# Performance work log

Measured on AMD Instinct MI355X. Metric: run time of the kernel, lower is better.

The kernel has to match this reference:

```python
import jax, jax.numpy as jnp
import numpy as np

HEADS = 16
HIDDEN = 1024
HEAD_DIM = HIDDEN // HEADS


def setup_inputs() -> dict:
    key = jax.random.key(0)
    ks = jax.random.split(key, 12)
    B, S, H = 2, 2048, HIDDEN
    scale = 1.0 / np.sqrt(H)
    inp = {
        'q': jax.random.normal(ks[0], (B, S, H), jnp.float32),
        'k': jax.random.normal(ks[1], (B, S, H), jnp.float32),
        'v': jax.random.normal(ks[2], (B, S, H), jnp.float32),
        'mask': jnp.ones((B, S), jnp.int32),
        'Wq': jax.random.normal(ks[3], (H, H), jnp.float32) * scale,
        'bq': jnp.zeros((H,), jnp.float32),
        'Wk': jax.random.normal(ks[4], (H, H), jnp.float32) * scale,
        'bk': jnp.zeros((H,), jnp.float32),
        'Wv': jax.random.normal(ks[5], (H, H), jnp.float32) * scale,
        'bv': jnp.zeros((H,), jnp.float32),
        'Wo': jax.random.normal(ks[6], (H, H), jnp.float32) * scale,
        'bo': jnp.zeros((H,), jnp.float32),
    }
    return inp


def reference(q, k, v, mask, Wq, bq, Wk, bk, Wv, bv, Wo, bo):
    B, S, H = q.shape
    hd = HEAD_DIM
    # projections (torch Linear: x @ W.T + b) -> [B, heads, S, hd]
    qh = (q @ Wq.T + bq).reshape(B, S, HEADS, hd).transpose(0, 2, 1, 3)
    kh = (k @ Wk.T + bk).reshape(B, S, HEADS, hd).transpose(0, 2, 1, 3)
    vh = (v @ Wv.T + bv).reshape(B, S, HEADS, hd).transpose(0, 2, 1, 3)
    # full score matrix [B, heads, Sq, Sk]
    scores = jnp.einsum('bhqd,bhkd->bhqk', qh, kh) / np.sqrt(hd)
    # mask [B, Sq] -> [B, 1, Sq, 1], masks entire query rows where mask==0
    m = mask[:, None, :, None]
    scores = jnp.where(m == 0, jnp.float32(-1e9), scores)
    attn = jax.nn.softmax(scores, axis=-1)
    # dropout omitted (eval mode / deterministic)
    y = jnp.einsum('bhqk,bhkd->bhqd', attn, vh)
    y = y.transpose(0, 2, 1, 3).reshape(B, S, H)
    return y @ Wo.T + bo
```

## Files before the change

kernel.cpp:

```cpp
#include <hip/hip_runtime.h>
#include <hip/hip_bf16.h>
#include <cstdint>

#define EL 1048576ull

typedef __bf16 bf16_t;
typedef bf16_t bf16x8 __attribute__((ext_vector_type(8)));
typedef float  f32x4  __attribute__((ext_vector_type(4)));
typedef unsigned int u32x2 __attribute__((ext_vector_type(2)));
typedef unsigned int u32x4 __attribute__((ext_vector_type(4)));

__device__ __forceinline__ unsigned short f2bf(float f) {
  unsigned int u = __builtin_bit_cast(unsigned int, f);
  u += 0x7FFFu + ((u >> 16) & 1u);
  return (unsigned short)(u >> 16);
}

__device__ __forceinline__ unsigned int cvtpk(float lo, float hi2) {
  unsigned int r;
  asm("v_cvt_pk_bf16_f32 %0, %1, %2" : "=v"(r) : "v"(lo), "v"(hi2));
  return r;
}

__device__ __forceinline__ float fexp2(float x) {
#if __has_builtin(__builtin_amdgcn_exp2f)
  return __builtin_amdgcn_exp2f(x);
#else
  return exp2f(x);
#endif
}

typedef __attribute__((address_space(1))) void as1_void;
typedef __attribute__((address_space(3))) void as3_void;
__device__ __forceinline__ void load_lds16(const void* g, void* l) {
  __builtin_amdgcn_global_load_lds((as1_void*)g, (as3_void*)l, 16, 0, 0);
}

__device__ __forceinline__ bf16x8 repack_af(const f32x4 s0v, const f32x4 s1v) {
  unsigned int c00 = cvtpk(s0v[0], s0v[1]);
  unsigned int c01 = cvtpk(s0v[2], s0v[3]);
  unsigned int c10 = cvtpk(s1v[0], s1v[1]);
  unsigned int c11 = cvtpk(s1v[2], s1v[3]);
  asm("v_permlane32_swap_b32 %0, %1" : "+v"(c00), "+v"(c10));
  asm("v_permlane16_swap_b32 %0, %1" : "+v"(c00), "+v"(c10));
  asm("v_permlane32_swap_b32 %0, %1" : "+v"(c01), "+v"(c11));
  asm("v_permlane16_swap_b32 %0, %1" : "+v"(c01), "+v"(c11));
  u32x4 wd; wd[0] = c00; wd[1] = c01; wd[2] = c10; wd[3] = c11;
  return __builtin_bit_cast(bf16x8, wd);
}

__global__ __launch_bounds__(256) void convert_all(
    const float* __restrict__ q, const float* __restrict__ k, const float* __restrict__ v,
    const float* __restrict__ wq, const float* __restrict__ wk,
    const float* __restrict__ wv, const float* __restrict__ wo,
    unsigned short* __restrict__ ws)
{
  const size_t total_v4 = 4 * EL;
  for (size_t v4 = (size_t)blockIdx.x * blockDim.x + threadIdx.x; v4 < total_v4;
       v4 += (size_t)gridDim.x * blockDim.x) {
    size_t e = v4 * 4;
    unsigned seg = (unsigned)(e >> 20);
    const float* s; size_t base;
    if      (seg < 4)   { s = q;  base = 0; }
    else if (seg < 8)   { s = k;  base = 4*EL; }
    else if (seg < 12)  { s = v;  base = 8*EL; }
    else if (seg == 12) { s = wq; base = 12*EL; }
    else if (seg == 13) { s = wk; base = 13*EL; }
    else if (seg == 14) { s = wv; base = 14*EL; }
    else                { s = wo; base = 15*EL; }
    const float4 f = *(const float4*)(s + (e - base));
    ushort4 o;
    o.x = f2bf(f.x); o.y = f2bf(f.y); o.z = f2bf(f.z); o.w = f2bf(f.w);
    *(ushort4*)(ws + e) = o;
  }
}

template <int BM, int BN, int WM, int WN>
__device__ __forceinline__ void gemm_bt_main(
    const unsigned short* __restrict__ A,
    const unsigned short* __restrict__ B,
    f32x4 (&acc)[BM / WM / 16][BN / WN / 16],
    const int tm, const int tn)
{
  constexpr int K = 1024, BK = 64;
  constexpr int AM = BM / WM / 16, AN = BN / WN / 16;
  __shared__ __align__(16) unsigned short sA[BM * BK];
  __shared__ __align__(16) unsigned short sB[BN * BK];
  const int tid  = threadIdx.x;
  const int wave = tid >> 6, lane = tid & 63;
  const int wm = wave / WN, wn = wave % WN;
  const int l16 = lane & 15, hi = lane >> 4, swz = l16 & 7;

  for (int k0 = 0; k0 < K; k0 += BK) {
    __syncthreads();
#pragma unroll
    for (int i = 0; i < BM * 8 / 256; i++) {
      int p = i * 256 + tid;
      int row = p >> 3, c = p & 7;
      load_lds16(A + (size_t)(tm + row) * K + k0 + ((c ^ (row & 7)) * 8),
                 &sA[(i * 256 + wave * 64) * 8]);
    }
#pragma unroll
    for (int i = 0; i < BN * 8 / 256; i++) {
      int p = i * 256 + tid;
      int row = p >> 3, c = p & 7;
      load_lds16(B + (size_t)(tn + row) * K + k0 + ((c ^ (row & 7)) * 8),
                 &sB[(i * 256 + wave * 64) * 8]);
    }
    __syncthreads();

#pragma unroll
    for (int kk = 0; kk < 2; kk++) {
      bf16x8 af[AM], bfr[AN];
#pragma unroll
      for (int i = 0; i < AM; i++) {
        int row = wm * (BM / WM) + i * 16 + l16;
        af[i] = *(const bf16x8*)&sA[row * BK + (((kk * 4 + hi) ^ swz) * 8)];
      }
#pragma unroll
      for (int j = 0; j < AN; j++) {
        int row = wn * (BN / WN) + j * 16 + l16;
        bfr[j] = *(const bf16x8*)&sB[row * BK + (((kk * 4 + hi) ^ swz) * 8)];
      }
#pragma unroll
      for (int i = 0; i < AM; i++)
#pragma unroll
        for (int j = 0; j < AN; j++)
          acc[i][j] = __builtin_amdgcn_mfma_f32_16x16x32_bf16(af[i], bfr[j], acc[i][j], 0, 0, 0);
    }
  }
}

__global__ __launch_bounds__(256, 3) void qkv_gemm(
    const unsigned short* qb, const unsigned short* kb, const unsigned short* vb,
    const unsigned short* wqb, const unsigned short* wkb, const unsigned short* wvb,
    const float* bq, const float* bk, const float* bv,
    unsigned short* Qp, unsigned short* Kp, unsigned short* Vt)
{
  const unsigned short* A; const unsigned short* B; const float* bias;
  if (blockIdx.z == 0)      { A = qb; B = wqb; bias = bq; }
  else if (blockIdx.z == 1) { A = kb; B = wkb; bias = bk; }
  else                      { A = vb; B = wvb; bias = bv; }

  const int xd = blockIdx.x, yd = blockIdx.y;
  const int mt = xd + 8 * (yd & 3);
  const int nt = yd >> 2;
  const int tm = mt * 128, tn = nt * 128;

  f32x4 acc[4][4] = {};
  gemm_bt_main<128, 128, 2, 2>(A, B, acc, tm, tn);

  const int tid = threadIdx.x, wave = tid >> 6, lane = tid & 63;
  const int wm = wave >> 1, wn = wave & 1;
  const int l16 = lane & 15, hi = lane >> 4;

  if (blockIdx.z < 2) {
    unsigned short* C = (blockIdx.z == 0) ? Qp : Kp;
    const float scale = (blockIdx.z == 0) ? 0.18033688011112042f : 1.0f;
#pragma unroll
    for (int i = 0; i < 4; i++) {
      int row0 = tm + wm * 64 + i * 16 + hi * 4;
#pragma unroll
      for (int j = 0; j < 4; j++) {
        int col = tn + wn * 64 + j * 16 + l16;
        float bv2 = bias[col];
#pragma unroll
        for (int r = 0; r < 4; r++)
          C[(size_t)(row0 + r) * 1024 + col] = f2bf((acc[i][j][r] + bv2) * scale);
      }
    }
  } else {
#pragma unroll
    for (int i = 0; i < 4; i++) {
      int row0 = tm + wm * 64 + i * 16 + hi * 4;
      int bb = row0 >> 11, s = row0 & 2047;
#pragma unroll
      for (int j = 0; j < 4; j++) {
        int col = tn + wn * 64 + j * 16 + l16;
        int hh = col >> 6, d = col & 63;
        float bv2 = bias[col];
        u32x2 w;
        w[0] = cvtpk(acc[i][j][0] + bv2, acc[i][j][1] + bv2);
        w[1] = cvtpk(acc[i][j][2] + bv2, acc[i][j][3] + bv2);
        *(u32x2*)&Vt[((size_t)(bb * 16 + hh) * 64 + d) * 2048 + s] = w;
      }
    }
  }
}

__global__ __launch_bounds__(256, 2) void out_gemm(
    const unsigned short* Yb, const unsigned short* wob, const float* bo, float* out)
{
  const int xd = blockIdx.x, yd = blockIdx.y;
  const int mt = (xd & 7) + 8 * (yd & 3);
  const int nt = (xd >> 3) + 2 * (yd >> 2);
  const int tm = mt * 128, tn = nt * 64;

  f32x4 acc[2][4] = {};
  gemm_bt_main<128, 64, 4, 1>(Yb, wob, acc, tm, tn);

  const int tid = threadIdx.x, wave = tid >> 6, lane = tid & 63;
  const int l16 = lane & 15, hi = lane >> 4;
#pragma unroll
  for (int i = 0; i < 2; i++) {
    int row0 = tm + wave * 32 + i * 16 + hi * 4;
#pragma unroll
    for (int j = 0; j < 4; j++) {
      int col = tn + j * 16 + l16;
      float bv2 = bo[col];
#pragma unroll
      for (int r = 0; r < 4; r++)
        out[(size_t)(row0 + r) * 1024 + col] = acc[i][j][r] + bv2;
    }
  }
}

__global__ __launch_bounds__(512, 2) void attn_kernel(
    const unsigned short* __restrict__ Qp, const unsigned short* __restrict__ Kp,
    const unsigned short* __restrict__ Vt, const int* __restrict__ mask,
    unsigned short* __restrict__ Yb)
{
  constexpr int S = 2048, H = 1024;
  __shared__ __align__(16) unsigned short smem[32768];

  const int tid = threadIdx.x, wave = tid >> 6, lane = tid & 63;
  const int l16 = lane & 15, hi = lane >> 4, swz = l16 & 7;
  const int half = wave >> 2, w4 = wave & 3;
  const int kvoff = half * 1024;
  const int xd = blockIdx.x, hd = blockIdx.y;
  const int h  = (xd & 7) + 8 * (hd & 1);
  const int qt = ((xd >> 3) + 2 * (hd >> 1)) * 128;
  const int b = blockIdx.z, bh = b * 16 + h;
  const unsigned short* Qb = Qp + (size_t)b * S * H + (size_t)h * 64;
  const unsigned short* Kb = Kp + (size_t)b * S * H + (size_t)h * 64;
  const unsigned short* Vb = Vt + (size_t)bh * 64 * 2048;

  unsigned short* sK0 = smem + (half * 2) * 4096;
  unsigned short* sK1 = smem + (half * 2 + 1) * 4096;
  unsigned short* sV0 = smem + 16384 + (half * 2) * 4096;
  unsigned short* sV1 = smem + 16384 + (half * 2 + 1) * 4096;

  const int kinv0 = l16 * 64 + ((hi ^ swz) * 8);
  const int kinv1 = l16 * 64 + (((4 + hi) ^ swz) * 8);
  const int vinv0 = kinv0, vinv1 = kinv1;

  {
    unsigned short* qdst0 = smem + 4096;
    unsigned short* qdst1 = smem + 12288;
#pragma unroll
    for (int i = 0; i < 2; i++) {
      int p = i * 512 + tid, row = p >> 3, c = p & 7;
      load_lds16(Qb + (size_t)(qt + row) * H + ((c ^ (row & 7)) * 8),
                 &(i ? qdst1 : qdst0)[(wave * 64) * 8]);
    }
  }
  const int htid = tid & 255;
  const unsigned short* pK[2]; const unsigned short* pV[2];
#pragma unroll
  for (int j = 0; j < 2; j++) {
    int g = j * 256 + htid;
    int row = g >> 3, c = g & 7;
    pK[j] = Kb + (size_t)(kvoff + row) * H + ((c ^ (row & 7)) * 8);
    int d = g >> 3, kvc = g & 7;
    int sg = kvc ^ (d & 7);
    pV[j] = Vb + (size_t)d * 2048 + kvoff + sg * 8;
  }
#pragma unroll
  for (int j = 0; j < 2; j++)
    load_lds16(pK[j], &sK0[(j * 256 + w4 * 64) * 8]);
#pragma unroll
  for (int j = 0; j < 2; j++)
    load_lds16(pV[j], &sV0[(j * 256 + w4 * 64) * 8]);
#pragma unroll
  for (int j = 0; j < 2; j++) { pK[j] += 64 * H; pV[j] += 64; }

  asm volatile("s_waitcnt vmcnt(4)" ::: "memory");
  __builtin_amdgcn_sched_barrier(0);
  __builtin_amdgcn_s_barrier();

  bf16x8 qf[2][2];
#pragma unroll
  for (int m = 0; m < 2; m++) {
    const int row = w4 * 32 + m * 16 + l16;
    const int qm = mask[(size_t)b * S + qt + row];
    const unsigned short* qsrc = (row < 64) ? (smem + 4096 + row * 64)
                                            : (smem + 12288 + (row - 64) * 64);
#pragma unroll
    for (int ks = 0; ks < 2; ks++) {
      bf16x8 v = *(const bf16x8*)&qsrc[((ks * 4 + hi) ^ swz) * 8];
      u32x4 u = __builtin_bit_cast(u32x4, v);
#pragma unroll
      for (int c = 0; c < 4; c++) u[c] = qm ? u[c] : 0u;
      qf[m][ks] = __builtin_bit_cast(bf16x8, u);
    }
  }
  asm volatile("s_waitcnt lgkmcnt(0)" ::: "memory");
  __builtin_amdgcn_sched_barrier(0);

  float lsum[2] = {0.f, 0.f};
  f32x4 oacc[2][4] = {};

  for (int t = 0; t < 16; t++) {
    const int cur = t & 1;
    asm volatile("s_waitcnt vmcnt(0)" ::: "memory");
    __builtin_amdgcn_sched_barrier(0);
    __builtin_amdgcn_s_barrier();

    if (t < 15) {
      unsigned short* nK = cur ? sK0 : sK1;
      unsigned short* nV = cur ? sV0 : sV1;
#pragma unroll
      for (int j = 0; j < 2; j++)
        load_lds16(pK[j], &nK[(j * 256 + w4 * 64) * 8]);
#pragma unroll
      for (int j = 0; j < 2; j++)
        load_lds16(pV[j], &nV[(j * 256 + w4 * 64) * 8]);
#pragma unroll
      for (int j = 0; j < 2; j++) { pK[j] += 64 * H; pV[j] += 64; }
    }

    const unsigned short* kb = cur ? sK1 : sK0;
    const unsigned short* vb = cur ? sV1 : sV0;

    f32x4 sf[2][4];
    __builtin_amdgcn_s_setprio(1);
#pragma unroll
    for (int jj = 0; jj < 4; jj++) {
      const int ro = jj * 1024;
      bf16x8 kf0 = *(const bf16x8*)&kb[ro + kinv0];
      bf16x8 kf1 = *(const bf16x8*)&kb[ro + kinv1];
#pragma unroll
      for (int m = 0; m < 2; m++) {
        f32x4 acc = {-16.0f, -16.0f, -16.0f, -16.0f};
        acc = __builtin_amdgcn_mfma_f32_16x16x32_bf16(kf0, qf[m][0], acc, 0, 0, 0);
        acc = __builtin_amdgcn_mfma_f32_16x16x32_bf16(kf1, qf[m][1], acc, 0, 0, 0);
        sf[m][jj] = acc;
      }
    }
    __builtin_amdgcn_s_setprio(0);

#pragma unroll
    for (int m = 0; m < 2; m++) {
#pragma unroll
      for (int jj = 0; jj < 4; jj++)
#pragma unroll
        for (int r = 0; r < 4; r++)
          sf[m][jj][r] = fexp2(sf[m][jj][r]);
      f32x4 c4 = (sf[m][0] + sf[m][1]) + (sf[m][2] + sf[m][3]);
      lsum[m] += (c4[0] + c4[1]) + (c4[2] + c4[3]);
    }

#pragma unroll
    for (int w2 = 0; w2 < 2; w2++) {
      bf16x8 af0 = repack_af(sf[0][2 * w2], sf[0][2 * w2 + 1]);
      bf16x8 af1 = repack_af(sf[1][2 * w2], sf[1][2 * w2 + 1]);
      const int vo = w2 ? vinv1 : vinv0;
      __builtin_amdgcn_s_setprio(1);
#pragma unroll
      for (int n = 0; n < 4; n++) {
        bf16x8 vf = *(const bf16x8*)&vb[n * 1024 + vo];
        oacc[0][n] = __builtin_amdgcn_mfma_f32_16x16x32_bf16(af0, vf, oacc[0][n], 0, 0, 0);
        oacc[1][n] = __builtin_amdgcn_mfma_f32_16x16x32_bf16(af1, vf, oacc[1][n], 0, 0, 0);
      }
      __builtin_amdgcn_s_setprio(0);
    }
  }

#pragma unroll
  for (int m = 0; m < 2; m++) {
    lsum[m] += __shfl_xor(lsum[m], 16);
    lsum[m] += __shfl_xor(lsum[m], 32);
  }

  __syncthreads();

  float* sO = (float*)smem;
  float* sL = (float*)(smem + 16896);

  if (half == 1) {
#pragma unroll
    for (int m = 0; m < 2; m++) {
      if (hi == 0) sL[w4 * 32 + m * 16 + l16] = lsum[m];
#pragma unroll
      for (int n = 0; n < 4; n++)
#pragma unroll
        for (int r = 0; r < 4; r++) {
          int qq = w4 * 32 + m * 16 + hi * 4 + r;
          sO[qq * 66 + n * 16 + l16] = oacc[m][n][r];
        }
    }
  }
  __syncthreads();
  if (half == 0) {
#pragma unroll
    for (int m = 0; m < 2; m++) {
      float lt = lsum[m] + sL[w4 * 32 + m * 16 + l16];
      float lr[4];
#pragma unroll
      for (int r = 0; r < 4; r++) lr[r] = 1.0f / __shfl(lt, hi * 4 + r);
#pragma unroll
      for (int n = 0; n < 4; n++)
#pragma unroll
        for (int r = 0; r < 4; r++) {
          int qq = w4 * 32 + m * 16 + hi * 4 + r;
          int col = n * 16 + l16;
          float val = (oacc[m][n][r] + sO[qq * 66 + col]) * lr[r];
          Yb[((size_t)b * S + qt + qq) * H + h * 64 + col] = f2bf(val);
        }
    }
  }
}

extern "C" void kernel_launch(void* const* d_in, const int* in_sizes, int n_in,
                              void* d_out, int out_size, void* d_ws, size_t ws_size,
                              hipStream_t stream)
{
  const float* q  = (const float*)d_in[0];
  const float* k  = (const float*)d_in[1];
  const float* v  = (const float*)d_in[2];
  const int*  mask = (const int*)d_in[3];
  const float* Wq = (const float*)d_in[4];
  const float* bq = (const float*)d_in[5];
  const float* Wk = (const float*)d_in[6];
  const float* bk = (const float*)d_in[7];
  const float* Wv = (const float*)d_in[8];
  const float* bv = (const float*)d_in[9];
  const float* Wo = (const float*)d_in[10];
  const float* bo = (const float*)d_in[11];

  unsigned short* ws  = (unsigned short*)d_ws;
  unsigned short* qb  = ws;
  unsigned short* kb  = ws + 4 * EL;
  unsigned short* vb  = ws + 8 * EL;
  unsigned short* wqb = ws + 12 * EL;
  unsigned short* wkb = ws + 13 * EL;
  unsigned short* wvb = ws + 14 * EL;
  unsigned short* wob = ws + 15 * EL;
  unsigned short* Qp  = ws + 16 * EL;
  unsigned short* Kp  = ws + 20 * EL;
  unsigned short* Vt  = ws + 24 * EL;
  unsigned short* Yb  = ws + 28 * EL;

  convert_all<<<2048, 256, 0, stream>>>(q, k, v, Wq, Wk, Wv, Wo, ws);
  qkv_gemm<<<dim3(8, 32, 3), 256, 0, stream>>>(qb, kb, vb, wqb, wkb, wvb,
                                               bq, bk, bv, Qp, Kp, Vt);
  attn_kernel<<<dim3(16, 16, 2), 512, 0, stream>>>(Qp, Kp, Vt, mask, Yb);
  out_gemm<<<dim3(16, 32), 256, 0, stream>>>(Yb, wob, bo, (float*)d_out);
}
```

Before: 104.1 us.

## Halve attention LDS footprint with 32-key tiles to raise occupancy

The attention kernel shrinks its shared-memory buffer from 64KB to 32KB by streaming 32-key K/V tiles instead of 64, doubling the loop trip count. It re-swizzles the V layout for the narrower tile, reuses the Q staging area, and splits the cross-half output reduction into two passes so it fits the smaller buffer. Launch bounds are raised so more blocks can be resident per CU. The aim is more latency hiding through occupancy, at the cost of more barriers per key, less MFMA work between syncs, and tighter register limits.

```diff
diff --git a/kernel.cpp b/kernel.cpp
--- a/kernel.cpp
+++ b/kernel.cpp
@@ -215,13 +215,13 @@
   }
 }
 
-__global__ __launch_bounds__(512, 2) void attn_kernel(
+__global__ __launch_bounds__(512, 6) void attn_kernel(
     const unsigned short* __restrict__ Qp, const unsigned short* __restrict__ Kp,
     const unsigned short* __restrict__ Vt, const int* __restrict__ mask,
     unsigned short* __restrict__ Yb)
 {
   constexpr int S = 2048, H = 1024;
-  __shared__ __align__(16) unsigned short smem[32768];
+  __shared__ __align__(16) unsigned short smem[16384];
 
   const int tid = threadIdx.x, wave = tid >> 6, lane = tid & 63;
   const int l16 = lane & 15, hi = lane >> 4, swz = l16 & 7;
@@ -235,106 +235,92 @@
   const unsigned short* Kb = Kp + (size_t)b * S * H + (size_t)h * 64;
   const unsigned short* Vb = Vt + (size_t)bh * 64 * 2048;
 
-  unsigned short* sK0 = smem + (half * 2) * 4096;
-  unsigned short* sK1 = smem + (half * 2 + 1) * 4096;
-  unsigned short* sV0 = smem + 16384 + (half * 2) * 4096;
-  unsigned short* sV1 = smem + 16384 + (half * 2 + 1) * 4096;
+  unsigned short* sK0 = smem + half * 4096;
+  unsigned short* sK1 = sK0 + 2048;
+  unsigned short* sV0 = smem + 8192 + half * 4096;
+  unsigned short* sV1 = sV0 + 2048;
 
   const int kinv0 = l16 * 64 + ((hi ^ swz) * 8);
   const int kinv1 = l16 * 64 + (((4 + hi) ^ swz) * 8);
-  const int vinv0 = kinv0, vinv1 = kinv1;
-
+  const int vinv  = l16 * 32 + ((hi ^ ((l16 >> 1) & 3)) * 8);
+
+#pragma unroll
+  for (int i = 0; i < 2; i++) {
+    const int g0 = i * 512 + wave * 64;
+    const int p = g0 + lane;
+    const int row = p >> 3, c = p & 7;
+    load_lds16(Qb + (size_t)(qt + row) * H + ((c ^ (row & 7)) * 8),
+               &smem[2048 + (g0 >> 8) * 4096 + (g0 & 255) * 8]);
+  }
+  const int htid = tid & 255;
+  const unsigned short* pK; const unsigned short* pV;
   {
-    unsigned short* qdst0 = smem + 4096;
-    unsigned short* qdst1 = smem + 12288;
-#pragma unroll
-    for (int i = 0; i < 2; i++) {
-      int p = i * 512 + tid, row = p >> 3, c = p & 7;
-      load_lds16(Qb + (size_t)(qt + row) * H + ((c ^ (row & 7)) * 8),
-                 &(i ? qdst1 : qdst0)[(wave * 64) * 8]);
-    }
-  }
-  const int htid = tid & 255;
-  const unsigned short* pK[2]; const unsigned short* pV[2];
-#pragma unroll
-  for (int j = 0; j < 2; j++) {
-    int g = j * 256 + htid;
-    int row = g >> 3, c = g & 7;
-    pK[j] = Kb + (size_t)(kvoff + row) * H + ((c ^ (row & 7)) * 8);
-    int d = g >> 3, kvc = g & 7;
-    int sg = kvc ^ (d & 7);
-    pV[j] = Vb + (size_t)d * 2048 + kvoff + sg * 8;
-  }
-#pragma unroll
-  for (int j = 0; j < 2; j++)
-    load_lds16(pK[j], &sK0[(j * 256 + w4 * 64) * 8]);
-#pragma unroll
-  for (int j = 0; j < 2; j++)
-    load_lds16(pV[j], &sV0[(j * 256 + w4 * 64) * 8]);
-#pragma unroll
-  for (int j = 0; j < 2; j++) { pK[j] += 64 * H; pV[j] += 64; }
-
-  asm volatile("s_waitcnt vmcnt(4)" ::: "memory");
+    int row = htid >> 3, c = htid & 7;
+    pK = Kb + (size_t)(kvoff + row) * H + ((c ^ (row & 7)) * 8);
+    int d = htid >> 2, kvc = htid & 3;
+    int sg = kvc ^ ((d >> 1) & 3);
+    pV = Vb + (size_t)d * 2048 + kvoff + sg * 8;
+  }
+  load_lds16(pK, &sK0[(w4 * 64) * 8]);
+  load_lds16(pV, &sV0[(w4 * 64) * 8]);
+  pK += 32 * H; pV += 32;
+
+  asm volatile("s_waitcnt vmcnt(2)" ::: "memory");
   __builtin_amdgcn_sched_barrier(0);
   __builtin_amdgcn_s_barrier();
 
   bf16x8 qf[2][2];
-#pragma unroll
-  for (int m = 0; m < 2; m++) {
-    const int row = w4 * 32 + m * 16 + l16;
-    const int qm = mask[(size_t)b * S + qt + row];
-    const unsigned short* qsrc = (row < 64) ? (smem + 4096 + row * 64)
-                                            : (smem + 12288 + (row - 64) * 64);
-#pragma unroll
-    for (int ks = 0; ks < 2; ks++) {
-      bf16x8 v = *(const bf16x8*)&qsrc[((ks * 4 + hi) ^ swz) * 8];
-      u32x4 u = __builtin_bit_cast(u32x4, v);
-#pragma unroll
-      for (int c = 0; c < 4; c++) u[c] = qm ? u[c] : 0u;
-      qf[m][ks] = __builtin_bit_cast(bf16x8, u);
+  {
+    const unsigned short* qreg = smem + 2048 + w4 * 4096;
+#pragma unroll
+    for (int m = 0; m < 2; m++) {
+      const int row = w4 * 32 + m * 16 + l16;
+      const int qm = mask[(size_t)b * S + qt + row];
+#pragma unroll
+      for (int ks = 0; ks < 2; ks++) {
+        bf16x8 v = *(const bf16x8*)&qreg[(m * 16 + l16) * 64 + (((ks * 4 + hi) ^ swz) * 8)];
+        u32x4 u = __builtin_bit_cast(u32x4, v);
+#pragma unroll
+        for (int c = 0; c < 4; c++) u[c] = qm ? u[c] : 0u;
+        qf[m][ks] = __builtin_bit_cast(bf16x8, u);
+      }
     }
   }
   asm volatile("s_waitcnt lgkmcnt(0)" ::: "memory");
   __builtin_amdgcn_sched_barrier(0);
 
+  const f32x4 c16 = {-16.0f, -16.0f, -16.0f, -16.0f};
   float lsum[2] = {0.f, 0.f};
   f32x4 oacc[2][4] = {};
 
-  for (int t = 0; t < 16; t++) {
+  for (int t = 0; t < 32; t++) {
     const int cur = t & 1;
     asm volatile("s_waitcnt vmcnt(0)" ::: "memory");
     __builtin_amdgcn_sched_barrier(0);
     __builtin_amdgcn_s_barrier();
 
-    if (t < 15) {
+    if (t < 31) {
       unsigned short* nK = cur ? sK0 : sK1;
       unsigned short* nV = cur ? sV0 : sV1;
-#pragma unroll
-      for (int j = 0; j < 2; j++)
-        load_lds16(pK[j], &nK[(j * 256 + w4 * 64) * 8]);
-#pragma unroll
-      for (int j = 0; j < 2; j++)
-        load_lds16(pV[j], &nV[(j * 256 + w4 * 64) * 8]);
-#pragma unroll
-      for (int j = 0; j < 2; j++) { pK[j] += 64 * H; pV[j] += 64; }
+      load_lds16(pK, &nK[(w4 * 64) * 8]);
+      load_lds16(pV, &nV[(w4 * 64) * 8]);
+      pK += 32 * H; pV += 32;
     }
 
     const unsigned short* kb = cur ? sK1 : sK0;
     const unsigned short* vb = cur ? sV1 : sV0;
 
-    f32x4 sf[2][4];
+    f32x4 sf[2][2];
     __builtin_amdgcn_s_setprio(1);
 #pragma unroll
-    for (int jj = 0; jj < 4; jj++) {
-      const int ro = jj * 1024;
+    for (int j = 0; j < 2; j++) {
+      const int ro = j * 1024;
       bf16x8 kf0 = *(const bf16x8*)&kb[ro + kinv0];
       bf16x8 kf1 = *(const bf16x8*)&kb[ro + kinv1];
 #pragma unroll
       for (int m = 0; m < 2; m++) {
-        f32x4 acc = {-16.0f, -16.0f, -16.0f, -16.0f};
-        acc = __builtin_amdgcn_mfma_f32_16x16x32_bf16(kf0, qf[m][0], acc, 0, 0, 0);
-        acc = __builtin_amdgcn_mfma_f32_16x16x32_bf16(kf1, qf[m][1], acc, 0, 0, 0);
-        sf[m][jj] = acc;
+        f32x4 a = __builtin_amdgcn_mfma_f32_16x16x32_bf16(kf0, qf[m][0], c16, 0, 0, 0);
+        sf[m][j] = __builtin_amdgcn_mfma_f32_16x16x32_bf16(kf1, qf[m][1], a, 0, 0, 0);
       }
     }
     __builtin_amdgcn_s_setprio(0);
@@ -342,23 +328,21 @@
 #pragma unroll
     for (int m = 0; m < 2; m++) {
 #pragma unroll
-      for (int jj = 0; jj < 4; jj++)
+      for (int j = 0; j < 2; j++)
 #pragma unroll
         for (int r = 0; r < 4; r++)
-          sf[m][jj][r] = fexp2(sf[m][jj][r]);
-      f32x4 c4 = (sf[m][0] + sf[m][1]) + (sf[m][2] + sf[m][3]);
+          sf[m][j][r] = fexp2(sf[m][j][r]);
+      f32x4 c4 = sf[m][0] + sf[m][1];
       lsum[m] += (c4[0] + c4[1]) + (c4[2] + c4[3]);
     }
 
-#pragma unroll
-    for (int w2 = 0; w2 < 2; w2++) {
-      bf16x8 af0 = repack_af(sf[0][2 * w2], sf[0][2 * w2 + 1]);
-      bf16x8 af1 = repack_af(sf[1][2 * w2], sf[1][2 * w2 + 1]);
-      const int vo = w2 ? vinv1 : vinv0;
+    {
+      bf16x8 af0 = repack_af(sf[0][0], sf[0][1]);
+      bf16x8 af1 = repack_af(sf[1][0], sf[1][1]);
       __builtin_amdgcn_s_setprio(1);
 #pragma unroll
       for (int n = 0; n < 4; n++) {
-        bf16x8 vf = *(const bf16x8*)&vb[n * 1024 + vo];
+        bf16x8 vf = *(const bf16x8*)&vb[n * 512 + vinv];
         oacc[0][n] = __builtin_amdgcn_mfma_f32_16x16x32_bf16(af0, vf, oacc[0][n], 0, 0, 0);
         oacc[1][n] = __builtin_amdgcn_mfma_f32_16x16x32_bf16(af1, vf, oacc[1][n], 0, 0, 0);
       }
@@ -375,39 +359,43 @@
   __syncthreads();
 
   float* sO = (float*)smem;
-  float* sL = (float*)(smem + 16896);
-
-  if (half == 1) {
-#pragma unroll
-    for (int m = 0; m < 2; m++) {
-      if (hi == 0) sL[w4 * 32 + m * 16 + l16] = lsum[m];
-#pragma unroll
-      for (int n = 0; n < 4; n++)
-#pragma unroll
-        for (int r = 0; r < 4; r++) {
-          int qq = w4 * 32 + m * 16 + hi * 4 + r;
-          sO[qq * 66 + n * 16 + l16] = oacc[m][n][r];
-        }
-    }
-  }
-  __syncthreads();
-  if (half == 0) {
-#pragma unroll
-    for (int m = 0; m < 2; m++) {
-      float lt = lsum[m] + sL[w4 * 32 + m * 16 + l16];
-      float lr[4];
-#pragma unroll
-      for (int r = 0; r < 4; r++) lr[r] = 1.0f / __shfl(lt, hi * 4 + r);
-#pragma unroll
-      for (int n = 0; n < 4; n++)
-#pragma unroll
-        for (int r = 0; r < 4; r++) {
-          int qq = w4 * 32 + m * 16 + hi * 4 + r;
-          int col = n * 16 + l16;
-          float val = (oacc[m][n][r] + sO[qq * 66 + col]) * lr[r];
-          Yb[((size_t)b * S + qt + qq) * H + h * 64 + col] = f2bf(val);
-        }
-    }
+  float* sL = (float*)smem + 64 * 66;
+
+#pragma unroll
+  for (int pass = 0; pass < 2; pass++) {
+    if (half == 1 && (w4 >> 1) == pass) {
+      const int lrow = (w4 & 1) * 32;
+#pragma unroll
+      for (int m = 0; m < 2; m++) {
+        if (hi == 0) sL[lrow + m * 16 + l16] = lsum[m];
+#pragma unroll
+        for (int n = 0; n < 4; n++)
+#pragma unroll
+          for (int r = 0; r < 4; r++)
+            sO[(lrow + m * 16 + hi * 4 + r) * 66 + n * 16 + l16] = oacc[m][n][r];
+      }
+    }
+    __syncthreads();
+    if (half == 0 && (w4 >> 1) == pass) {
+      const int lrow = (w4 & 1) * 32;
+#pragma unroll
+      for (int m = 0; m < 2; m++) {
+        float lt = lsum[m] + sL[lrow + m * 16 + l16];
+        float lr[4];
+#pragma unroll
+        for (int r = 0; r < 4; r++) lr[r] = 1.0f / __shfl(lt, hi * 4 + r);
+#pragma unroll
+        for (int n = 0; n < 4; n++)
+#pragma unroll
+          for (int r = 0; r < 4; r++) {
+            int lq = lrow + m * 16 + hi * 4 + r;
+            int col = n * 16 + l16;
+            float val = (oacc[m][n][r] + sO[lq * 66 + col]) * lr[r];
+            Yb[((size_t)b * S + qt + pass * 64 + lq) * H + h * 64 + col] = f2bf(val);
+          }
+      }
+    }
+    __syncthreads();
   }
 }
 
```

After: 145.7 us. 1.4x slower.
